# Kernel optimization log

Hardware: AMD Instinct MI355X
Metric: run time of the kernel (lower is better)

Reference implementation:

```python
import jax, jax.numpy as jnp
import numpy as np

LN_EPS = 1e-5


def setup_inputs() -> dict:
    key = jax.random.key(0)
    ks = jax.random.split(key, 4)
    B, N, C, K = 512, 100, 256, 3
    query = jax.random.normal(ks[0], (B, N, C), dtype=jnp.float32)
    value = jax.random.normal(ks[1], (B, N, C), dtype=jnp.float32)
    # nn.Linear(C, N+K): weight stored as [out,in] in torch; here use [in,out]
    W_wl = jax.random.normal(ks[2], (C, N + K), dtype=jnp.float32) / np.sqrt(C)
    b_wl = jax.random.normal(ks[3], (N + K,), dtype=jnp.float32) * 0.01
    ln_gamma = jnp.ones((C,), dtype=jnp.float32)
    ln_beta = jnp.zeros((C,), dtype=jnp.float32)
    return {"query": query, "value": value, "W_wl": W_wl, "b_wl": b_wl,
            "ln_gamma": ln_gamma, "ln_beta": ln_beta}


def reference(query, value, W_wl, b_wl, ln_gamma, ln_beta):
    B, N, C = query.shape
    K = W_wl.shape[1] - N
    # dynamic conv weights from query: [B, N, K] depthwise + [B, N, N] pointwise
    dy = jnp.einsum('bnc,ck->bnk', query, W_wl) + b_wl
    dw = dy[:, :, :K]          # depthwise kernels, one per (b, proposal)
    pw = dy[:, :, K:]          # pointwise mixing matrix [B, N, N]
    # depthwise conv1d along C with 'same' padding (cross-correlation like torch)
    pad_l = (K - 1) // 2
    pad_r = K - 1 - pad_l
    vp = jnp.pad(value, ((0, 0), (0, 0), (pad_l, pad_r)))
    depth = jnp.zeros_like(value)
    for k in range(K):  # K is tiny (3): static unrolled loop
        depth = depth + dw[:, :, k:k + 1] * vp[:, :, k:k + C]
    depth = jax.nn.relu(depth)
    # pointwise conv (kernel size 1) == per-sample NxN mix over proposals
    out = jnp.einsum('bnm,bmc->bnc', pw, depth)
    # LayerNorm over C
    mu = jnp.mean(out, axis=-1, keepdims=True)
    var = jnp.var(out, axis=-1, keepdims=True)
    out = (out - mu) * jax.lax.rsqrt(var + LN_EPS) * ln_gamma + ln_beta
    return out
```

## Files before the change

kernel.cpp:

```cpp
#include <hip/hip_runtime.h>

#define NN 100
#define CC 256
#define NKK 103
#define LDPW 136
#define OTS 260

typedef __bf16 bf16;
typedef __bf16 bf16x8 __attribute__((ext_vector_type(8)));
typedef float f32x4 __attribute__((ext_vector_type(4)));

__global__ void wl_transpose(const float* __restrict__ W, bf16* __restrict__ Wt)
{
    int idx = blockIdx.x * 256 + threadIdx.x;
    if (idx < NKK * CC) {
        int ka = idx >> 8;
        int k  = idx & 255;
        Wt[ka * CC + k] = (bf16)W[k * NKK + ka];
    }
}

__global__ __launch_bounds__(256, 2)
void dysepconv_fused(const float* __restrict__ query,
                     const float* __restrict__ value,
                     const bf16*  __restrict__ Wt,
                     const float* __restrict__ bwl,
                     const float* __restrict__ gamma,
                     const float* __restrict__ beta,
                     float* __restrict__ out)
{
    __shared__ __align__(16) char SMEM[52800];
    bf16*  PW = (bf16*)SMEM;
    float (*DW)[3]     = (float(*)[3])(SMEM + 27200);
    float (*RP)[NN][2] = (float(*)[NN][2])(SMEM + 28400);
    float (*RS)[2]     = (float(*)[2])(SMEM + 52000);
    float* OT = (float*)SMEM;

    const int t    = threadIdx.x;
    const int w    = t >> 6;
    const int lane = t & 63;
    const int ln16 = lane & 15;
    const int g    = lane >> 4;
    const int hi8  = g * 8;
    const int b    = blockIdx.x;
    const int cb0  = w * 16 + ln16;

    const float* qb = query + (size_t)b * NN * CC;
    const float* vb = value + (size_t)b * NN * CC;

    f32x4 acc1[2][7];
    #pragma unroll
    for (int u = 0; u < 2; ++u)
        #pragma unroll
        for (int J = 0; J < 7; ++J) acc1[u][J] = (f32x4){0.f, 0.f, 0.f, 0.f};

    #pragma unroll
    for (int u = 0; u < 2; ++u) {
        if (u == 0 || w < 3) {
            const int tile = w + u * 4;
            const int qrow = (tile * 16 + ln16 < NN) ? (tile * 16 + ln16) : (NN - 1);
            const float* qr = qb + qrow * CC;
            #pragma unroll
            for (int kc = 0; kc < 4; ++kc) {
                bf16x8 qf[2];
                #pragma unroll
                for (int s = 0; s < 2; ++s) {
                    f32x4 a0 = *(const f32x4*)(qr + kc * 64 + s * 32 + hi8);
                    f32x4 a1 = *(const f32x4*)(qr + kc * 64 + s * 32 + hi8 + 4);
                    #pragma unroll
                    for (int i = 0; i < 4; ++i) { qf[s][i] = (bf16)a0[i]; qf[s][i + 4] = (bf16)a1[i]; }
                }
                #pragma unroll
                for (int J = 0; J < 7; ++J) {
                    const int rB = (J * 16 + ln16 < NKK) ? (J * 16 + ln16) : (NKK - 1);
                    bf16x8 bv0 = *(const bf16x8*)(Wt + rB * CC + kc * 64 + hi8);
                    bf16x8 bv1 = *(const bf16x8*)(Wt + rB * CC + kc * 64 + 32 + hi8);
                    acc1[u][J] = __builtin_amdgcn_mfma_f32_16x16x32_bf16(qf[0], bv0, acc1[u][J], 0, 0, 0);
                    acc1[u][J] = __builtin_amdgcn_mfma_f32_16x16x32_bf16(qf[1], bv1, acc1[u][J], 0, 0, 0);
                }
            }
        }
    }

    for (int i = t; i < NN * 28; i += 256) {
        int r = i / 28, m = 100 + (i - (i / 28) * 28);
        PW[r * LDPW + m] = (bf16)0.f;
    }
    float xv[4][8];
    #pragma unroll
    for (int s = 0; s < 4; ++s)
        #pragma unroll
        for (int j = 0; j < 8; ++j) {
            int m = hi8 + j;
            xv[s][j] = vb[m * CC + cb0 + 64 * s];
        }
    #pragma unroll
    for (int u = 0; u < 2; ++u) {
        if (u == 0 || w < 3) {
            #pragma unroll
            for (int J = 0; J < 7; ++J) {
                int kap = J * 16 + ln16;
                float bw = (kap < NKK) ? bwl[kap] : 0.f;
                #pragma unroll
                for (int r = 0; r < 4; ++r) {
                    int n = (w + u * 4) * 16 + g * 4 + r;
                    if (n < NN && kap < NKK) {
                        float v = acc1[u][J][r] + bw;
                        if (kap < 3) DW[n][kap] = v;
                        else         PW[n * LDPW + (kap - 3)] = (bf16)v;
                    }
                }
            }
        }
    }
    __syncthreads();

    f32x4 acc2[4][7];
    #pragma unroll
    for (int s = 0; s < 4; ++s)
        #pragma unroll
        for (int I = 0; I < 7; ++I) acc2[s][I] = (f32x4){0.f, 0.f, 0.f, 0.f};

    #pragma unroll
    for (int ks = 0; ks < 4; ++ks) {
        if (ks) {
            #pragma unroll
            for (int s = 0; s < 4; ++s)
                #pragma unroll
                for (int j = 0; j < 8; ++j) {
                    int m = ks * 32 + hi8 + j;
                    bool mv = (m < NN);
                    xv[s][j] = mv ? vb[m * CC + cb0 + 64 * s] : 0.f;
                }
        }
        bf16x8 dv[4];
        #pragma unroll
        for (int j = 0; j < 8; ++j) {
            int  m  = ks * 32 + hi8 + j;
            bool mv = (m < NN);
            int  mc = mv ? m : (NN - 1);
            float w0 = DW[mc][0], w1 = DW[mc][1], w2 = DW[mc][2];
            #pragma unroll
            for (int s = 0; s < 4; ++s) {
                int c = cb0 + 64 * s;
                float x0 = xv[s][j];
                float xm = __shfl(x0, (lane - 1) & 63);
                float xp = __shfl(x0, (lane + 1) & 63);
                if (ln16 == 0)  xm = (mv && c > 0)      ? vb[m * CC + c - 1] : 0.f;
                if (ln16 == 15) xp = (mv && c + 1 < CC) ? vb[m * CC + c + 1] : 0.f;
                float d = w0 * xm + w1 * x0 + w2 * xp;
                dv[s][j] = (bf16)(mv ? fmaxf(d, 0.f) : 0.f);
            }
        }
        #pragma unroll
        for (int I = 0; I < 7; ++I) {
            int row = I * 16 + ln16;
            row = (row < NN) ? row : (NN - 1);
            bf16x8 af = *(const bf16x8*)&PW[row * LDPW + ks * 32 + hi8];
            #pragma unroll
            for (int s = 0; s < 4; ++s)
                acc2[s][I] = __builtin_amdgcn_mfma_f32_16x16x32_bf16(af, dv[s], acc2[s][I], 0, 0, 0);
        }
    }

    float gm[4], bt[4];
    #pragma unroll
    for (int s = 0; s < 4; ++s) { gm[s] = gamma[cb0 + 64 * s]; bt[s] = beta[cb0 + 64 * s]; }

    #pragma unroll
    for (int I = 0; I < 7; ++I) {
        #pragma unroll
        for (int r = 0; r < 4; ++r) {
            float s1 = 0.f, s2 = 0.f;
            #pragma unroll
            for (int s = 0; s < 4; ++s) {
                float a = acc2[s][I][r];
                s1 += a; s2 += a * a;
            }
            #pragma unroll
            for (int mk = 1; mk < 16; mk <<= 1) {
                s1 += __shfl_xor(s1, mk);
                s2 += __shfl_xor(s2, mk);
            }
            int n = I * 16 + g * 4 + r;
            if (ln16 == 0 && n < NN) {
                RP[w][n][0] = s1;
                RP[w][n][1] = s2;
            }
        }
    }
    __syncthreads();
    if (t < NN) {
        float S1 = 0.f, S2 = 0.f;
        #pragma unroll
        for (int wi = 0; wi < 4; ++wi) { S1 += RP[wi][t][0]; S2 += RP[wi][t][1]; }
        float mu  = S1 * (1.f / 256.f);
        float var = S2 * (1.f / 256.f) - mu * mu;
        RS[t][0] = mu;
        RS[t][1] = rsqrtf(fmaxf(var, 0.f) + 1e-5f);
    }
    __syncthreads();

    float* ob = out + (size_t)b * NN * CC;
    #pragma unroll
    for (int h = 0; h < 2; ++h) {
        const int n0 = h * 50;
        #pragma unroll
        for (int I = 0; I < 7; ++I) {
            #pragma unroll
            for (int r = 0; r < 4; ++r) {
                int n = I * 16 + g * 4 + r;
                if (n >= n0 && n < n0 + 50 && n < NN) {
                    float mu = RS[n][0], rs = RS[n][1];
                    int rt = n - n0;
                    #pragma unroll
                    for (int s = 0; s < 4; ++s)
                        OT[rt * OTS + cb0 + 64 * s] = (acc2[s][I][r] - mu) * rs * gm[s] + bt[s];
                }
            }
        }
        __syncthreads();
        #pragma unroll
        for (int p = 0; p < 13; ++p) {
            int idx = p * 256 + t;
            if (idx < 50 * 64) {
                int row = idx >> 6, c4 = (idx & 63) << 2;
                *(f32x4*)(ob + (size_t)(n0 + row) * CC + c4) = *(const f32x4*)&OT[row * OTS + c4];
            }
        }
        if (h == 0) __syncthreads();
    }
}

extern "C" void kernel_launch(void* const* d_in, const int* in_sizes, int n_in,
                              void* d_out, int out_size, void* d_ws, size_t ws_size,
                              hipStream_t stream) {
    const float* query = (const float*)d_in[0];
    const float* value = (const float*)d_in[1];
    const float* W     = (const float*)d_in[2];
    const float* bwl   = (const float*)d_in[3];
    const float* gamma = (const float*)d_in[4];
    const float* beta  = (const float*)d_in[5];
    bf16* Wt = (bf16*)d_ws;

    wl_transpose<<<dim3((NKK * CC + 255) / 256), dim3(256), 0, stream>>>(W, Wt);
    dysepconv_fused<<<dim3(512), dim3(256), 0, stream>>>(query, value, Wt, bwl, gamma, beta, (float*)d_out);
}
```

Baseline: 184.5 us.

## Preload query fragments, stage conv halos in LDS, prefetch next value chunk

Restructures the first GEMM so each wave converts its query rows to bf16 fragments once, then loops over weight tiles so each Wt fragment load feeds both row tiles. Border values for the depthwise conv are staged into an LDS halo table instead of being fetched with per-lane global loads inside the inner loop. The value chunk for the next k-step is prefetched while the current chunk is processed, overlapping global latency with compute. The cost is higher register pressure (qfr, xn) under a launch bound of two blocks, which risks spilling.

```diff
diff --git a/kernel.cpp b/kernel.cpp
--- a/kernel.cpp
+++ b/kernel.cpp
@@ -5,6 +5,7 @@
 #define NKK 103
 #define LDPW 136
 #define OTS 260
+#define LHALO 34
 
 typedef __bf16 bf16;
 typedef __bf16 bf16x8 __attribute__((ext_vector_type(8)));
@@ -31,9 +32,10 @@
 {
     __shared__ __align__(16) char SMEM[52800];
     bf16*  PW = (bf16*)SMEM;
-    float (*DW)[3]     = (float(*)[3])(SMEM + 27200);
-    float (*RP)[NN][2] = (float(*)[NN][2])(SMEM + 28400);
-    float (*RS)[2]     = (float(*)[2])(SMEM + 52000);
+    float (*DW)[3]      = (float(*)[3])(SMEM + 27200);
+    float (*RP)[NN][2]  = (float(*)[NN][2])(SMEM + 28400);
+    float (*HALO)[LHALO]= (float(*)[LHALO])(SMEM + 31600);
+    float (*RS)[2]      = (float(*)[2])(SMEM + 52000);
     float* OT = (float*)SMEM;
 
     const int t    = threadIdx.x;
@@ -48,40 +50,55 @@
     const float* qb = query + (size_t)b * NN * CC;
     const float* vb = value + (size_t)b * NN * CC;
 
+    const int nt = (w < 3) ? 2 : 1;
+
     f32x4 acc1[2][7];
     #pragma unroll
     for (int u = 0; u < 2; ++u)
         #pragma unroll
         for (int J = 0; J < 7; ++J) acc1[u][J] = (f32x4){0.f, 0.f, 0.f, 0.f};
 
+    bf16x8 qfr[2][8];
     #pragma unroll
     for (int u = 0; u < 2; ++u) {
-        if (u == 0 || w < 3) {
+        if (u < nt) {
             const int tile = w + u * 4;
             const int qrow = (tile * 16 + ln16 < NN) ? (tile * 16 + ln16) : (NN - 1);
             const float* qr = qb + qrow * CC;
             #pragma unroll
-            for (int kc = 0; kc < 4; ++kc) {
-                bf16x8 qf[2];
-                #pragma unroll
-                for (int s = 0; s < 2; ++s) {
-                    f32x4 a0 = *(const f32x4*)(qr + kc * 64 + s * 32 + hi8);
-                    f32x4 a1 = *(const f32x4*)(qr + kc * 64 + s * 32 + hi8 + 4);
-                    #pragma unroll
-                    for (int i = 0; i < 4; ++i) { qf[s][i] = (bf16)a0[i]; qf[s][i + 4] = (bf16)a1[i]; }
-                }
-                #pragma unroll
-                for (int J = 0; J < 7; ++J) {
-                    const int rB = (J * 16 + ln16 < NKK) ? (J * 16 + ln16) : (NKK - 1);
-                    bf16x8 bv0 = *(const bf16x8*)(Wt + rB * CC + kc * 64 + hi8);
-                    bf16x8 bv1 = *(const bf16x8*)(Wt + rB * CC + kc * 64 + 32 + hi8);
-                    acc1[u][J] = __builtin_amdgcn_mfma_f32_16x16x32_bf16(qf[0], bv0, acc1[u][J], 0, 0, 0);
-                    acc1[u][J] = __builtin_amdgcn_mfma_f32_16x16x32_bf16(qf[1], bv1, acc1[u][J], 0, 0, 0);
-                }
-            }
-        }
-    }
-
+            for (int f = 0; f < 8; ++f) {
+                const int col = (f >> 1) * 64 + (f & 1) * 32 + hi8;
+                f32x4 a0 = *(const f32x4*)(qr + col);
+                f32x4 a1 = *(const f32x4*)(qr + col + 4);
+                #pragma unroll
+                for (int i = 0; i < 4; ++i) { qfr[u][f][i] = (bf16)a0[i]; qfr[u][f][i + 4] = (bf16)a1[i]; }
+            }
+        }
+    }
+
+    #pragma unroll
+    for (int J = 0; J < 7; ++J) {
+        const int rB = (J * 16 + ln16 < NKK) ? (J * 16 + ln16) : (NKK - 1);
+        const bf16* wr = Wt + rB * CC;
+        bf16x8 bv[8];
+        #pragma unroll
+        for (int f = 0; f < 8; ++f)
+            bv[f] = *(const bf16x8*)(wr + (f >> 1) * 64 + (f & 1) * 32 + hi8);
+        #pragma unroll
+        for (int u = 0; u < 2; ++u) {
+            if (u < nt) {
+                #pragma unroll
+                for (int f = 0; f < 8; ++f)
+                    acc1[u][J] = __builtin_amdgcn_mfma_f32_16x16x32_bf16(qfr[u][f], bv[f], acc1[u][J], 0, 0, 0);
+            }
+        }
+    }
+
+    for (int i = t; i < NN * 32; i += 256) {
+        int m = i >> 5, k = i & 31;
+        int col = (k & 1) ? (16 * ((k + 1) >> 1)) : (16 * (k >> 1) - 1);
+        HALO[m][k] = (col >= 0 && col < CC) ? vb[m * CC + col] : 0.f;
+    }
     for (int i = t; i < NN * 28; i += 256) {
         int r = i / 28, m = 100 + (i - (i / 28) * 28);
         PW[r * LDPW + m] = (bf16)0.f;
@@ -96,7 +113,7 @@
         }
     #pragma unroll
     for (int u = 0; u < 2; ++u) {
-        if (u == 0 || w < 3) {
+        if (u < nt) {
             #pragma unroll
             for (int J = 0; J < 7; ++J) {
                 int kap = J * 16 + ln16;
@@ -123,14 +140,15 @@
 
     #pragma unroll
     for (int ks = 0; ks < 4; ++ks) {
-        if (ks) {
+        float xn[4][8];
+        if (ks < 3) {
             #pragma unroll
             for (int s = 0; s < 4; ++s)
                 #pragma unroll
                 for (int j = 0; j < 8; ++j) {
-                    int m = ks * 32 + hi8 + j;
+                    int m = (ks + 1) * 32 + hi8 + j;
                     bool mv = (m < NN);
-                    xv[s][j] = mv ? vb[m * CC + cb0 + 64 * s] : 0.f;
+                    xn[s][j] = mv ? vb[m * CC + cb0 + 64 * s] : 0.f;
                 }
         }
         bf16x8 dv[4];
@@ -142,12 +160,12 @@
             float w0 = DW[mc][0], w1 = DW[mc][1], w2 = DW[mc][2];
             #pragma unroll
             for (int s = 0; s < 4; ++s) {
-                int c = cb0 + 64 * s;
                 float x0 = xv[s][j];
                 float xm = __shfl(x0, (lane - 1) & 63);
                 float xp = __shfl(x0, (lane + 1) & 63);
-                if (ln16 == 0)  xm = (mv && c > 0)      ? vb[m * CC + c - 1] : 0.f;
-                if (ln16 == 15) xp = (mv && c + 1 < CC) ? vb[m * CC + c + 1] : 0.f;
+                const int i0 = w + 4 * s;
+                if (ln16 == 0)  xm = HALO[mc][2 * i0];
+                if (ln16 == 15) xp = HALO[mc][2 * i0 + 1];
                 float d = w0 * xm + w1 * x0 + w2 * xp;
                 dv[s][j] = (bf16)(mv ? fmaxf(d, 0.f) : 0.f);
             }
@@ -160,6 +178,12 @@
             #pragma unroll
             for (int s = 0; s < 4; ++s)
                 acc2[s][I] = __builtin_amdgcn_mfma_f32_16x16x32_bf16(af, dv[s], acc2[s][I], 0, 0, 0);
+        }
+        if (ks < 3) {
+            #pragma unroll
+            for (int s = 0; s < 4; ++s)
+                #pragma unroll
+                for (int j = 0; j < 8; ++j) xv[s][j] = xn[s][j];
         }
     }
 
```

New measurement: 216.7 us. 1.17x slower.

## Split fused kernel into separate query GEMM and conv/GEMM2/LayerNorm kernels

Applied to the files above, without the earlier changes.

The single fused kernel is split in two. The first kernel runs the query projection GEMM across 800 blocks over flattened rows and writes the pointwise weights (bf16) and depthwise weights into the output buffer as scratch. The second kernel uses 512 threads per block: it computes the depthwise conv into a transposed shared tile, then each wave owns 16 full rows of the pointwise GEMM, so LayerNorm statistics are reduced within the wave without a cross-wave shared reduction. The aim is more parallelism for GEMM1 and less synchronisation, at the cost of an extra launch and a global round trip for the dynamic weights.

```diff
diff --git a/kernel.cpp b/kernel.cpp
--- a/kernel.cpp
+++ b/kernel.cpp
@@ -3,12 +3,13 @@
 #define NN 100
 #define CC 256
 #define NKK 103
-#define LDPW 136
-#define OTS 260
+#define LDT 136
+#define OTS 264
 
 typedef __bf16 bf16;
 typedef __bf16 bf16x8 __attribute__((ext_vector_type(8)));
 typedef float f32x4 __attribute__((ext_vector_type(4)));
+
 
 __global__ void wl_transpose(const float* __restrict__ W, bf16* __restrict__ Wt)
 {
@@ -20,20 +21,76 @@
     }
 }
 
-__global__ __launch_bounds__(256, 2)
-void dysepconv_fused(const float* __restrict__ query,
-                     const float* __restrict__ value,
-                     const bf16*  __restrict__ Wt,
-                     const float* __restrict__ bwl,
-                     const float* __restrict__ gamma,
-                     const float* __restrict__ beta,
-                     float* __restrict__ out)
+__global__ __launch_bounds__(256, 4)
+void gemm1(const float* __restrict__ query, const bf16* __restrict__ Wt,
+           const float* __restrict__ bwl, float* __restrict__ out)
 {
-    __shared__ __align__(16) char SMEM[52800];
-    bf16*  PW = (bf16*)SMEM;
-    float (*DW)[3]     = (float(*)[3])(SMEM + 27200);
-    float (*RP)[NN][2] = (float(*)[NN][2])(SMEM + 28400);
-    float (*RS)[2]     = (float(*)[2])(SMEM + 52000);
+    const int t    = threadIdx.x;
+    const int w    = t >> 6;
+    const int lane = t & 63;
+    const int ln16 = lane & 15;
+    const int g    = lane >> 4;
+    const int hi8  = g * 8;
+    const int R0   = blockIdx.x * 64 + w * 16;
+
+    const float* qr = query + (size_t)(R0 + ln16) * CC;
+    bf16x8 qfr[8];
+    #pragma unroll
+    for (int f = 0; f < 8; ++f) {
+        const int col = f * 32 + hi8;
+        f32x4 a0 = *(const f32x4*)(qr + col);
+        f32x4 a1 = *(const f32x4*)(qr + col + 4);
+        #pragma unroll
+        for (int i = 0; i < 4; ++i) { qfr[f][i] = (bf16)a0[i]; qfr[f][i + 4] = (bf16)a1[i]; }
+    }
+
+    f32x4 acc[7];
+    #pragma unroll
+    for (int J = 0; J < 7; ++J) acc[J] = (f32x4){0.f, 0.f, 0.f, 0.f};
+
+    #pragma unroll
+    for (int J = 0; J < 7; ++J) {
+        const int rB = (J * 16 + ln16 < NKK) ? (J * 16 + ln16) : (NKK - 1);
+        const bf16* wr = Wt + rB * CC;
+        #pragma unroll
+        for (int f = 0; f < 8; ++f) {
+            bf16x8 bv = *(const bf16x8*)(wr + f * 32 + hi8);
+            acc[J] = __builtin_amdgcn_mfma_f32_16x16x32_bf16(qfr[f], bv, acc[J], 0, 0, 0);
+        }
+    }
+
+    int bb[4], nr[4];
+    #pragma unroll
+    for (int r = 0; r < 4; ++r) {
+        int nf = R0 + g * 4 + r;
+        bb[r] = nf / 100;
+        nr[r] = nf - bb[r] * 100;
+    }
+    #pragma unroll
+    for (int J = 0; J < 7; ++J) {
+        int kap = J * 16 + ln16;
+        float bw = (kap < NKK) ? bwl[kap] : 0.f;
+        #pragma unroll
+        for (int r = 0; r < 4; ++r) {
+            float v = acc[J][r] + bw;
+            float* base = out + (size_t)bb[r] * 25600;
+            if (kap >= 3 && kap < NKK)
+                ((bf16*)base)[nr[r] * 128 + (kap - 3)] = (bf16)v;
+            else if (kap < 3)
+                base[6400 + nr[r] * 4 + kap] = v;
+        }
+    }
+}
+
+__global__ __launch_bounds__(512, 4)
+void conv_gemm2_ln(const float* __restrict__ value,
+                   const float* __restrict__ gamma,
+                   const float* __restrict__ beta,
+                   float* __restrict__ out)
+{
+    __shared__ __align__(16) char SMEM[71232];
+    bf16* depthT = (bf16*)SMEM;
+    float (*DWs)[4] = (float(*)[4])(SMEM + 69632);
     float* OT = (float*)SMEM;
 
     const int t    = threadIdx.x;
@@ -43,106 +100,42 @@
     const int g    = lane >> 4;
     const int hi8  = g * 8;
     const int b    = blockIdx.x;
-    const int cb0  = w * 16 + ln16;
-
-    const float* qb = query + (size_t)b * NN * CC;
-    const float* vb = value + (size_t)b * NN * CC;
-
-    f32x4 acc1[2][7];
-    #pragma unroll
-    for (int u = 0; u < 2; ++u)
-        #pragma unroll
-        for (int J = 0; J < 7; ++J) acc1[u][J] = (f32x4){0.f, 0.f, 0.f, 0.f};
-
-    #pragma unroll
-    for (int u = 0; u < 2; ++u) {
-        if (u == 0 || w < 3) {
-            const int tile = w + u * 4;
-            const int qrow = (tile * 16 + ln16 < NN) ? (tile * 16 + ln16) : (NN - 1);
-            const float* qr = qb + qrow * CC;
-            #pragma unroll
-            for (int kc = 0; kc < 4; ++kc) {
-                bf16x8 qf[2];
-                #pragma unroll
-                for (int s = 0; s < 2; ++s) {
-                    f32x4 a0 = *(const f32x4*)(qr + kc * 64 + s * 32 + hi8);
-                    f32x4 a1 = *(const f32x4*)(qr + kc * 64 + s * 32 + hi8 + 4);
-                    #pragma unroll
-                    for (int i = 0; i < 4; ++i) { qf[s][i] = (bf16)a0[i]; qf[s][i + 4] = (bf16)a1[i]; }
-                }
-                #pragma unroll
-                for (int J = 0; J < 7; ++J) {
-                    const int rB = (J * 16 + ln16 < NKK) ? (J * 16 + ln16) : (NKK - 1);
-                    bf16x8 bv0 = *(const bf16x8*)(Wt + rB * CC + kc * 64 + hi8);
-                    bf16x8 bv1 = *(const bf16x8*)(Wt + rB * CC + kc * 64 + 32 + hi8);
-                    acc1[u][J] = __builtin_amdgcn_mfma_f32_16x16x32_bf16(qf[0], bv0, acc1[u][J], 0, 0, 0);
-                    acc1[u][J] = __builtin_amdgcn_mfma_f32_16x16x32_bf16(qf[1], bv1, acc1[u][J], 0, 0, 0);
-                }
-            }
-        }
-    }
-
-    for (int i = t; i < NN * 28; i += 256) {
-        int r = i / 28, m = 100 + (i - (i / 28) * 28);
-        PW[r * LDPW + m] = (bf16)0.f;
-    }
-    float xv[4][8];
-    #pragma unroll
-    for (int s = 0; s < 4; ++s)
-        #pragma unroll
-        for (int j = 0; j < 8; ++j) {
-            int m = hi8 + j;
-            xv[s][j] = vb[m * CC + cb0 + 64 * s];
-        }
-    #pragma unroll
-    for (int u = 0; u < 2; ++u) {
-        if (u == 0 || w < 3) {
-            #pragma unroll
-            for (int J = 0; J < 7; ++J) {
-                int kap = J * 16 + ln16;
-                float bw = (kap < NKK) ? bwl[kap] : 0.f;
-                #pragma unroll
-                for (int r = 0; r < 4; ++r) {
-                    int n = (w + u * 4) * 16 + g * 4 + r;
-                    if (n < NN && kap < NKK) {
-                        float v = acc1[u][J][r] + bw;
-                        if (kap < 3) DW[n][kap] = v;
-                        else         PW[n * LDPW + (kap - 3)] = (bf16)v;
-                    }
-                }
-            }
-        }
-    }
+    const int cb   = w * 16 + ln16;
+
+    float* ob = out + (size_t)b * 25600;
+    const bf16*  pwb = (const bf16*)ob;
+    const float* vb  = value + (size_t)b * NN * CC;
+
+    if (t < 400) ((float*)DWs)[t] = ob[6400 + t];
+    float xv[2][8];
+    #pragma unroll
+    for (int s = 0; s < 2; ++s)
+        #pragma unroll
+        for (int j = 0; j < 8; ++j)
+            xv[s][j] = vb[(hi8 + j) * CC + cb + 128 * s];
     __syncthreads();
-
-    f32x4 acc2[4][7];
-    #pragma unroll
-    for (int s = 0; s < 4; ++s)
-        #pragma unroll
-        for (int I = 0; I < 7; ++I) acc2[s][I] = (f32x4){0.f, 0.f, 0.f, 0.f};
 
     #pragma unroll
     for (int ks = 0; ks < 4; ++ks) {
         if (ks) {
             #pragma unroll
-            for (int s = 0; s < 4; ++s)
+            for (int s = 0; s < 2; ++s)
                 #pragma unroll
                 for (int j = 0; j < 8; ++j) {
                     int m = ks * 32 + hi8 + j;
-                    bool mv = (m < NN);
-                    xv[s][j] = mv ? vb[m * CC + cb0 + 64 * s] : 0.f;
+                    xv[s][j] = (m < NN) ? vb[m * CC + cb + 128 * s] : 0.f;
                 }
         }
-        bf16x8 dv[4];
+        bf16x8 dv[2];
         #pragma unroll
         for (int j = 0; j < 8; ++j) {
             int  m  = ks * 32 + hi8 + j;
             bool mv = (m < NN);
             int  mc = mv ? m : (NN - 1);
-            float w0 = DW[mc][0], w1 = DW[mc][1], w2 = DW[mc][2];
-            #pragma unroll
-            for (int s = 0; s < 4; ++s) {
-                int c = cb0 + 64 * s;
+            float w0 = DWs[mc][0], w1 = DWs[mc][1], w2 = DWs[mc][2];
+            #pragma unroll
+            for (int s = 0; s < 2; ++s) {
+                int c = cb + 128 * s;
                 float x0 = xv[s][j];
                 float xm = __shfl(x0, (lane - 1) & 63);
                 float xp = __shfl(x0, (lane + 1) & 63);
@@ -153,79 +146,73 @@
             }
         }
         #pragma unroll
-        for (int I = 0; I < 7; ++I) {
-            int row = I * 16 + ln16;
-            row = (row < NN) ? row : (NN - 1);
-            bf16x8 af = *(const bf16x8*)&PW[row * LDPW + ks * 32 + hi8];
-            #pragma unroll
-            for (int s = 0; s < 4; ++s)
-                acc2[s][I] = __builtin_amdgcn_mfma_f32_16x16x32_bf16(af, dv[s], acc2[s][I], 0, 0, 0);
-        }
-    }
-
-    float gm[4], bt[4];
-    #pragma unroll
-    for (int s = 0; s < 4; ++s) { gm[s] = gamma[cb0 + 64 * s]; bt[s] = beta[cb0 + 64 * s]; }
-
-    #pragma unroll
-    for (int I = 0; I < 7; ++I) {
+        for (int s = 0; s < 2; ++s)
+            *(bf16x8*)&depthT[(cb + 128 * s) * LDT + ks * 32 + hi8] = dv[s];
+    }
+    __syncthreads();
+
+    f32x4 acc[16];
+    #pragma unroll
+    for (int ct = 0; ct < 16; ++ct) acc[ct] = (f32x4){0.f, 0.f, 0.f, 0.f};
+    float mu[4], rs[4];
+
+    if (w < 7) {
+        const int arow = (w * 16 + ln16 < NN) ? (w * 16 + ln16) : (NN - 1);
+        bf16x8 av[4];
+        #pragma unroll
+        for (int ks = 0; ks < 4; ++ks)
+            av[ks] = *(const bf16x8*)(pwb + arow * 128 + ks * 32 + hi8);
+        #pragma unroll
+        for (int j = 0; j < 8; ++j)
+            av[3][j] = (96 + hi8 + j < NN) ? av[3][j] : (bf16)0.f;
+
+        #pragma unroll
+        for (int ct = 0; ct < 16; ++ct) {
+            #pragma unroll
+            for (int ks = 0; ks < 4; ++ks) {
+                bf16x8 bv = *(const bf16x8*)&depthT[(ct * 16 + ln16) * LDT + ks * 32 + hi8];
+                acc[ct] = __builtin_amdgcn_mfma_f32_16x16x32_bf16(av[ks], bv, acc[ct], 0, 0, 0);
+            }
+        }
         #pragma unroll
         for (int r = 0; r < 4; ++r) {
             float s1 = 0.f, s2 = 0.f;
             #pragma unroll
-            for (int s = 0; s < 4; ++s) {
-                float a = acc2[s][I][r];
-                s1 += a; s2 += a * a;
-            }
+            for (int ct = 0; ct < 16; ++ct) { float a = acc[ct][r]; s1 += a; s2 += a * a; }
             #pragma unroll
             for (int mk = 1; mk < 16; mk <<= 1) {
                 s1 += __shfl_xor(s1, mk);
                 s2 += __shfl_xor(s2, mk);
             }
-            int n = I * 16 + g * 4 + r;
-            if (ln16 == 0 && n < NN) {
-                RP[w][n][0] = s1;
-                RP[w][n][1] = s2;
-            }
+            float m_ = s1 * (1.f / 256.f);
+            float v_ = s2 * (1.f / 256.f) - m_ * m_;
+            mu[r] = m_;
+            rs[r] = rsqrtf(fmaxf(v_, 0.f) + 1e-5f);
         }
     }
     __syncthreads();
-    if (t < NN) {
-        float S1 = 0.f, S2 = 0.f;
-        #pragma unroll
-        for (int wi = 0; wi < 4; ++wi) { S1 += RP[wi][t][0]; S2 += RP[wi][t][1]; }
-        float mu  = S1 * (1.f / 256.f);
-        float var = S2 * (1.f / 256.f) - mu * mu;
-        RS[t][0] = mu;
-        RS[t][1] = rsqrtf(fmaxf(var, 0.f) + 1e-5f);
-    }
-    __syncthreads();
-
-    float* ob = out + (size_t)b * NN * CC;
+
     #pragma unroll
     for (int h = 0; h < 2; ++h) {
-        const int n0 = h * 50;
-        #pragma unroll
-        for (int I = 0; I < 7; ++I) {
-            #pragma unroll
-            for (int r = 0; r < 4; ++r) {
-                int n = I * 16 + g * 4 + r;
-                if (n >= n0 && n < n0 + 50 && n < NN) {
-                    float mu = RS[n][0], rs = RS[n][1];
-                    int rt = n - n0;
-                    #pragma unroll
-                    for (int s = 0; s < 4; ++s)
-                        OT[rt * OTS + cb0 + 64 * s] = (acc2[s][I][r] - mu) * rs * gm[s] + bt[s];
-                }
+        if (w >= 4 * h && w < 4 * h + 4 && w < 7) {
+            const int slot = w - 4 * h;
+            #pragma unroll
+            for (int ct = 0; ct < 16; ++ct) {
+                const float gmv = gamma[ct * 16 + ln16], btv = beta[ct * 16 + ln16];
+                #pragma unroll
+                for (int r = 0; r < 4; ++r)
+                    OT[(slot * 16 + g * 4 + r) * OTS + ct * 16 + ln16] =
+                        (acc[ct][r] - mu[r]) * rs[r] * gmv + btv;
             }
         }
         __syncthreads();
-        #pragma unroll
-        for (int p = 0; p < 13; ++p) {
-            int idx = p * 256 + t;
-            if (idx < 50 * 64) {
+        const int rows = h ? 36 : 64;
+        #pragma unroll
+        for (int p = 0; p < 8; ++p) {
+            int idx = p * 512 + t;
+            if (idx < rows * 64) {
                 int row = idx >> 6, c4 = (idx & 63) << 2;
-                *(f32x4*)(ob + (size_t)(n0 + row) * CC + c4) = *(const f32x4*)&OT[row * OTS + c4];
+                *(f32x4*)(ob + (size_t)(64 * h + row) * CC + c4) = *(const f32x4*)&OT[row * OTS + c4];
             }
         }
         if (h == 0) __syncthreads();
@@ -241,8 +228,10 @@
     const float* bwl   = (const float*)d_in[3];
     const float* gamma = (const float*)d_in[4];
     const float* beta  = (const float*)d_in[5];
+    float* out = (float*)d_out;
     bf16* Wt = (bf16*)d_ws;
 
     wl_transpose<<<dim3((NKK * CC + 255) / 256), dim3(256), 0, stream>>>(W, Wt);
-    dysepconv_fused<<<dim3(512), dim3(256), 0, stream>>>(query, value, Wt, bwl, gamma, beta, (float*)d_out);
-}
+    gemm1<<<dim3(800), dim3(256), 0, stream>>>(query, Wt, bwl, out);
+    conv_gemm2_ln<<<dim3(512), dim3(512), 0, stream>>>(value, gamma, beta, out);
+}
```

Result: no change. 186.3 us (+1.0%).
